# Kernel tuning notes

Measured on AMD Instinct MI355X. Metric: run time of the kernel, lower is better.

The kernel has to match this reference:

```python
import jax, jax.numpy as jnp
import numpy as np

DIM = 384
H = 6
D = DIM // H
MLP = 4 * DIM
SCALE = D ** -0.5
LN_EPS = 1e-5


def _ln(x, w, b):
    m = jnp.mean(x, axis=-1, keepdims=True)
    v = jnp.mean((x - m) ** 2, axis=-1, keepdims=True)
    return (x - m) * jax.lax.rsqrt(v + LN_EPS) * w + b


def setup_inputs() -> dict:
    key = jax.random.key(0)
    ks = jax.random.split(key, 8)
    B, N = 8, 1024
    x = jax.random.normal(ks[0], (B, N, DIM), dtype=jnp.float32)
    # torch nn.Linear weights are [out, in]
    qkv_w = jax.random.normal(ks[1], (3 * DIM, DIM), dtype=jnp.float32) * (DIM ** -0.5)
    proj_w = jax.random.normal(ks[2], (DIM, DIM), dtype=jnp.float32) * (DIM ** -0.5)
    proj_b = jnp.zeros((DIM,), jnp.float32)
    # L2Q params, 'quadratic' init
    alpha = jnp.full((H, 1, 1), 0.125, jnp.float32)
    beta = jnp.full((H, 1, 1), 0.5, jnp.float32)
    gamma = jnp.zeros((H, 1, 1), jnp.float32)
    ln1_w = jnp.ones((DIM,), jnp.float32)
    ln1_b = jnp.zeros((DIM,), jnp.float32)
    ln2_w = jnp.ones((DIM,), jnp.float32)
    ln2_b = jnp.zeros((DIM,), jnp.float32)
    w1 = jax.random.normal(ks[3], (MLP, DIM), dtype=jnp.float32) * (DIM ** -0.5)
    b1 = jnp.zeros((MLP,), jnp.float32)
    w2 = jax.random.normal(ks[4], (DIM, MLP), dtype=jnp.float32) * (MLP ** -0.5)
    b2 = jnp.zeros((DIM,), jnp.float32)
    return {"x": x, "qkv_w": qkv_w, "proj_w": proj_w, "proj_b": proj_b,
            "alpha": alpha, "beta": beta, "gamma": gamma,
            "ln1_w": ln1_w, "ln1_b": ln1_b, "ln2_w": ln2_w, "ln2_b": ln2_b,
            "w1": w1, "b1": b1, "w2": w2, "b2": b2}


def reference(x, qkv_w, proj_w, proj_b, alpha, beta, gamma,
              ln1_w, ln1_b, ln2_w, ln2_b, w1, b1, w2, b2):
    B, N, C = x.shape
    # --- L2Q attention on LN(x) ---
    h = _ln(x, ln1_w, ln1_b)
    qkv = (h @ qkv_w.T).reshape(B, N, 3, H, D)
    q = qkv[:, :, 0].transpose(0, 2, 1, 3)  # [B,H,N,D]
    k = qkv[:, :, 1].transpose(0, 2, 1, 3)
    v = qkv[:, :, 2].transpose(0, 2, 1, 3)
    logits = jnp.einsum('bhnd,bhmd->bhnm', q, k) * SCALE
    attn = jax.nn.relu(alpha * logits ** 2 + beta * logits + gamma)
    attn = attn / (jnp.sum(attn, axis=-1, keepdims=True) + 1e-6)
    out = jnp.einsum('bhnm,bhmd->bhnd', attn, v)
    out = out.transpose(0, 2, 1, 3).reshape(B, N, C)
    x = x + out @ proj_w.T + proj_b
    # --- MLP on LN(x), exact GELU (torch default) ---
    h2 = _ln(x, ln2_w, ln2_b)
    m = jax.nn.gelu(h2 @ w1.T + b1, approximate=False)
    x = x + m @ w2.T + b2
    return x
```

## Files before the change

kernel.cpp:

```cpp
#include <hip/hip_runtime.h>
#include <hip/hip_bf16.h>
#include <math.h>

#define DIMC 384
#define NH 6
#define HD 64
#define MLPD 1536
#define BS 8
#define SEQ 1024
#define T_TOK (BS*SEQ)
#define TC ((size_t)T_TOK*DIMC)
#define QK_SCALE 0.125f

typedef __bf16 bf16;
typedef bf16 bf16x4 __attribute__((ext_vector_type(4)));
typedef bf16 bf16x8 __attribute__((ext_vector_type(8)));
typedef float floatx4 __attribute__((ext_vector_type(4)));

__device__ __forceinline__ void async_cp16(const void* gsrc, void* ldst) {
    __builtin_amdgcn_global_load_lds(
        (const __attribute__((address_space(1))) unsigned int*)gsrc,
        (__attribute__((address_space(3))) unsigned int*)ldst,
        16, 0, 0);
}

__global__ __launch_bounds__(256)
void prep_kernel(const float* __restrict__ s0, const float* __restrict__ s1,
                 const float* __restrict__ s2, const float* __restrict__ s3,
                 bf16* __restrict__ dst,
                 const float* __restrict__ x, const float* __restrict__ lw,
                 const float* __restrict__ lb, bf16* __restrict__ out) {
    if (blockIdx.x < 1728) {
        int i = blockIdx.x * 256 + threadIdx.x;
        const int n0 = 110592, n1 = 36864, n2 = 147456;
        const float4* src; int j;
        if (i < n0)           { src = (const float4*)s0; j = i; }
        else if (i < n0+n1)   { src = (const float4*)s1; j = i - n0; }
        else if (i < n0+n1+n2){ src = (const float4*)s2; j = i - n0 - n1; }
        else                  { src = (const float4*)s3; j = i - n0 - n1 - n2; }
        float4 v = src[j];
        bf16x4 o; o[0] = (bf16)v.x; o[1] = (bf16)v.y; o[2] = (bf16)v.z; o[3] = (bf16)v.w;
        ((bf16x4*)dst)[i] = o;
    } else {
        int row = (blockIdx.x - 1728) * 4 + (threadIdx.x >> 6);
        int t = threadIdx.x & 63;
        const float* xr = x + (size_t)row * DIMC;
        float vals[6];
        float s = 0.f;
        #pragma unroll
        for (int i = 0; i < 6; i++) { vals[i] = xr[t + i*64]; s += vals[i]; }
        #pragma unroll
        for (int m = 32; m; m >>= 1) s += __shfl_xor(s, m);
        float mean = s * (1.0f / DIMC);
        float sq = 0.f;
        #pragma unroll
        for (int i = 0; i < 6; i++) { float d = vals[i] - mean; sq += d * d; }
        #pragma unroll
        for (int m = 32; m; m >>= 1) sq += __shfl_xor(sq, m);
        float rstd = rsqrtf(sq * (1.0f / DIMC) + 1e-5f);
        bf16* orow = out + (size_t)row * DIMC;
        #pragma unroll
        for (int i = 0; i < 6; i++) {
            int c = t + i*64;
            orow[c] = (bf16)((vals[i] - mean) * rstd * lw[c] + lb[c]);
        }
    }
}

__global__ __launch_bounds__(256)
void ln2_fused(const float* __restrict__ x, const bf16* __restrict__ p0,
               const bf16* __restrict__ p1, const float* __restrict__ pb,
               const float* __restrict__ w, const float* __restrict__ b,
               float* __restrict__ x1, bf16* __restrict__ h) {
    int row = blockIdx.x * 4 + (threadIdx.x >> 6);
    int t = threadIdx.x & 63;
    size_t base = (size_t)row * DIMC;
    float vals[6];
    float s = 0.f;
    #pragma unroll
    for (int i = 0; i < 6; i++) {
        int c = t + i*64;
        float v = x[base + c] + (float)p0[base + c] + (float)p1[base + c] + pb[c];
        vals[i] = v; s += v;
    }
    #pragma unroll
    for (int m = 32; m; m >>= 1) s += __shfl_xor(s, m);
    float mean = s * (1.0f / DIMC);
    float sq = 0.f;
    #pragma unroll
    for (int i = 0; i < 6; i++) { float d = vals[i] - mean; sq += d * d; }
    #pragma unroll
    for (int m = 32; m; m >>= 1) sq += __shfl_xor(sq, m);
    float rstd = rsqrtf(sq * (1.0f / DIMC) + 1e-5f);
    #pragma unroll
    for (int i = 0; i < 6; i++) {
        int c = t + i*64;
        x1[base + c] = vals[i];
        h[base + c] = (bf16)((vals[i] - mean) * rstd * w[c] + b[c]);
    }
}

__global__ __launch_bounds__(256)
void reduce4(float* __restrict__ xo, const bf16* __restrict__ p0, const bf16* __restrict__ p1,
             const bf16* __restrict__ p2, const bf16* __restrict__ p3,
             const float* __restrict__ b2) {
    int i = blockIdx.x * 256 + threadIdx.x;
    float4 v = ((const float4*)xo)[i];
    int c = (i % 96) * 4;
    float4 bb = *(const float4*)(b2 + c);
    bf16x4 a0 = ((const bf16x4*)p0)[i], a1 = ((const bf16x4*)p1)[i];
    bf16x4 a2 = ((const bf16x4*)p2)[i], a3 = ((const bf16x4*)p3)[i];
    v.x += bb.x + (float)a0[0] + (float)a1[0] + (float)a2[0] + (float)a3[0];
    v.y += bb.y + (float)a0[1] + (float)a1[1] + (float)a2[1] + (float)a3[1];
    v.z += bb.z + (float)a0[2] + (float)a1[2] + (float)a2[2] + (float)a3[2];
    v.w += bb.w + (float)a0[3] + (float)a1[3] + (float)a2[3] + (float)a3[3];
    ((float4*)xo)[i] = v;
}

enum { EPI_NONE = 0, EPI_QKV = 1, EPI_GELU = 3 };

template<int EPI, int K, int KS, typename OutT>
__global__ __launch_bounds__(256)
void gemm_bt(const bf16* __restrict__ A, const bf16* __restrict__ W,
             const float* __restrict__ bias, OutT* out, int M, int N) {
    __shared__ __align__(16) bf16 Ash[128*32];
    __shared__ __align__(16) bf16 Bsh[128*32];
    constexpr int KB = K / KS;
    int tid = threadIdx.x;
    int lane = tid & 63, w = tid >> 6;
    int quad = lane >> 4, l16 = lane & 15;
    int rbase = blockIdx.y * 128 + (w >> 1) * 64;
    int cbase = blockIdx.x * 128 + (w & 1) * 64;
    int kbase = blockIdx.z * KB;
    int c1 = w * 64 + lane;
    int c2 = c1 + 256;
    const bf16* Ag1 = A + (size_t)(blockIdx.y*128 + (c1 >> 2)) * K + kbase + (c1 & 3) * 8;
    const bf16* Ag2 = A + (size_t)(blockIdx.y*128 + (c2 >> 2)) * K + kbase + (c2 & 3) * 8;
    const bf16* Wg1 = W + (size_t)(blockIdx.x*128 + (c1 >> 2)) * K + kbase + (c1 & 3) * 8;
    const bf16* Wg2 = W + (size_t)(blockIdx.x*128 + (c2 >> 2)) * K + kbase + (c2 & 3) * 8;
    bf16* As1 = Ash + c1 * 8;  bf16* As2 = Ash + c2 * 8;
    bf16* Bs1 = Bsh + c1 * 8;  bf16* Bs2 = Bsh + c2 * 8;

    int arow = (w >> 1) * 64;
    int brow = (w & 1) * 64;
    floatx4 acc[4][4] = {};
    #pragma unroll
    for (int kk = 0; kk < KB / 32; kk++) {
        __syncthreads();
        async_cp16(Ag1 + kk*32, As1);
        async_cp16(Ag2 + kk*32, As2);
        async_cp16(Wg1 + kk*32, Bs1);
        async_cp16(Wg2 + kk*32, Bs2);
        __syncthreads();
        bf16x8 a[4], bfr[4];
        #pragma unroll
        for (int tm = 0; tm < 4; tm++)
            a[tm] = *(const bf16x8*)&Ash[(arow + tm*16 + l16) * 32 + quad*8];
        #pragma unroll
        for (int tn = 0; tn < 4; tn++)
            bfr[tn] = *(const bf16x8*)&Bsh[(brow + tn*16 + l16) * 32 + quad*8];
        #pragma unroll
        for (int tm = 0; tm < 4; tm++)
            #pragma unroll
            for (int tn = 0; tn < 4; tn++)
                acc[tm][tn] = __builtin_amdgcn_mfma_f32_16x16x32_bf16(a[tm], bfr[tn], acc[tm][tn], 0, 0, 0);
    }

    #pragma unroll
    for (int tm = 0; tm < 4; tm++)
        #pragma unroll
        for (int tn = 0; tn < 4; tn++) {
            if constexpr (EPI == EPI_QKV) {
                int colb = cbase + tn*16 + l16;
                int which = colb / 384;
                int rowb = rbase + tm*16 + quad*4;
                int bb = rowb >> 10;
                if (which == 2) {
                    int rem = colb - 768;
                    int hh = rem >> 6, d = rem & 63;
                    int n = rowb & 1023;
                    bf16x4 pk;
                    #pragma unroll
                    for (int r = 0; r < 4; r++) pk[r] = (bf16)acc[tm][tn][r];
                    *(bf16x4*)((bf16*)out + 2*TC + (((size_t)(bb*NH + hh) * HD + d) << 10) + n) = pk;
                } else {
                    int rem = colb - which*384;
                    int hh = rem >> 6, d = rem & 63;
                    #pragma unroll
                    for (int r = 0; r < 4; r++) {
                        int n = (rowb & 1023) + r;
                        ((bf16*)out)[(size_t)which*TC + (((size_t)(bb*NH + hh) * SEQ + n) << 6) + d]
                            = (bf16)acc[tm][tn][r];
                    }
                }
            } else if constexpr (EPI == EPI_NONE) {
                OutT* ob = out + (size_t)blockIdx.z * M * N;
                #pragma unroll
                for (int r = 0; r < 4; r++) {
                    int row = rbase + tm*16 + quad*4 + r;
                    int col = cbase + tn*16 + l16;
                    ob[(size_t)row * N + col] = (OutT)acc[tm][tn][r];
                }
            } else {
                #pragma unroll
                for (int r = 0; r < 4; r++) {
                    int row = rbase + tm*16 + quad*4 + r;
                    int col = cbase + tn*16 + l16;
                    float v = acc[tm][tn][r] + bias[col];
                    v = 0.5f * v * (1.0f + erff(v * 0.70710678118f));
                    out[(size_t)row * N + col] = (OutT)v;
                }
            }
        }
}

__global__ __launch_bounds__(256)
void attn_kernel(const bf16* __restrict__ q, const bf16* __restrict__ k,
                 const bf16* __restrict__ vt, const float* __restrict__ alpha,
                 const float* __restrict__ beta, const float* __restrict__ gamma,
                 bf16* __restrict__ attn_out) {
    __shared__ __align__(16) bf16 Psh[64][260];
    __shared__ float rsW[4][64];
    __shared__ float rs_final[64];

    int L = blockIdx.x;
    int xcd = L & 7, slot = L >> 3;
    int qt = slot & 15;
    int bh = xcd + ((slot >> 4) << 3);
    int bb = bh / NH, h = bh % NH;
    int q0 = qt * 64;
    int tid = threadIdx.x;
    int w = tid >> 6, lane = tid & 63, quad = lane >> 4, l16 = lane & 15;
    float av = alpha[h] * (QK_SCALE * QK_SCALE), bv = beta[h] * QK_SCALE, gv = gamma[h];
    const bf16* qb  = q  + (size_t)bh * SEQ * HD;
    const bf16* kb  = k  + (size_t)bh * SEQ * HD;
    const bf16* vtb = vt + (size_t)bh * HD * SEQ;

    floatx4 o[4] = {};
    float rsp[4] = {0.f, 0.f, 0.f, 0.f};

    bf16x8 kf[2][4], vf[8];
    #pragma unroll
    for (int ks = 0; ks < 2; ks++)
        #pragma unroll
        for (int ksub = 0; ksub < 4; ksub++)
            kf[ks][ksub] = *(const bf16x8*)(kb + (size_t)(w*64 + ksub*16 + l16) * HD + ks*32 + quad*8);
    const bf16* vrow = vtb + (size_t)(w*16 + l16) * SEQ;
    #pragma unroll
    for (int ksl = 0; ksl < 8; ksl++)
        vf[ksl] = *(const bf16x8*)(vrow + ksl*32 + quad*8);

    for (int c = 0; c < 4; c++) {
        #pragma unroll
        for (int qsub = 0; qsub < 4; qsub++) {
            bf16x8 qa0 = *(const bf16x8*)(qb + (size_t)(q0 + qsub*16 + l16) * HD + quad*8);
            bf16x8 qa1 = *(const bf16x8*)(qb + (size_t)(q0 + qsub*16 + l16) * HD + 32 + quad*8);
            floatx4 s[4] = {};
            #pragma unroll
            for (int ksub = 0; ksub < 4; ksub++)
                s[ksub] = __builtin_amdgcn_mfma_f32_16x16x32_bf16(kf[0][ksub], qa0, s[ksub], 0, 0, 0);
            #pragma unroll
            for (int ksub = 0; ksub < 4; ksub++)
                s[ksub] = __builtin_amdgcn_mfma_f32_16x16x32_bf16(kf[1][ksub], qa1, s[ksub], 0, 0, 0);
            #pragma unroll
            for (int ksub = 0; ksub < 4; ksub++) {
                bf16x4 p4;
                float rsum = 0.f;
                #pragma unroll
                for (int r = 0; r < 4; r++) {
                    float xx = s[ksub][r];
                    float p = fmaxf((av*xx + bv)*xx + gv, 0.f);
                    p4[r] = (bf16)p;
                    rsum += p;
                }
                rsp[qsub] += rsum;
                *(bf16x4*)&Psh[qsub*16 + l16][w*64 + ksub*16 + quad*4] = p4;
            }
        }
        __syncthreads();
        if (c < 3) {
            int kc = (c+1)*256 + w*64;
            #pragma unroll
            for (int ks = 0; ks < 2; ks++)
                #pragma unroll
                for (int ksub = 0; ksub < 4; ksub++)
                    kf[ks][ksub] = *(const bf16x8*)(kb + (size_t)(kc + ksub*16 + l16) * HD + ks*32 + quad*8);
        }
        #pragma unroll
        for (int ksl = 0; ksl < 8; ksl++) {
            #pragma unroll
            for (int qsub = 0; qsub < 4; qsub++) {
                bf16x4 plo = *(const bf16x4*)&Psh[qsub*16 + l16][ksl*32 + quad*8];
                bf16x4 phi = *(const bf16x4*)&Psh[qsub*16 + l16][ksl*32 + quad*8 + 4];
                bf16x8 pf = __builtin_shufflevector(plo, phi, 0, 1, 2, 3, 4, 5, 6, 7);
                o[qsub] = __builtin_amdgcn_mfma_f32_16x16x32_bf16(pf, vf[ksl], o[qsub], 0, 0, 0);
            }
        }
        if (c < 3) {
            const bf16* vr2 = vrow + (c+1)*256;
            #pragma unroll
            for (int ksl = 0; ksl < 8; ksl++)
                vf[ksl] = *(const bf16x8*)(vr2 + ksl*32 + quad*8);
        }
        __syncthreads();
    }

    #pragma unroll
    for (int qsub = 0; qsub < 4; qsub++) {
        rsp[qsub] += __shfl_xor(rsp[qsub], 16);
        rsp[qsub] += __shfl_xor(rsp[qsub], 32);
    }
    if (quad == 0) {
        #pragma unroll
        for (int qsub = 0; qsub < 4; qsub++)
            rsW[w][qsub*16 + l16] = rsp[qsub];
    }
    __syncthreads();
    if (tid < 64)
        rs_final[tid] = rsW[0][tid] + rsW[1][tid] + rsW[2][tid] + rsW[3][tid] + 1e-6f;
    __syncthreads();

    #pragma unroll
    for (int qsub = 0; qsub < 4; qsub++)
        #pragma unroll
        for (int r = 0; r < 4; r++) {
            int ql = qsub*16 + quad*4 + r;
            float rv = rs_final[ql];
            int n = q0 + ql;
            attn_out[((size_t)(bb*SEQ + n)) * DIMC + h*HD + w*16 + l16] =
                (bf16)(o[qsub][r] / rv);
        }
}

extern "C" void kernel_launch(void* const* d_in, const int* in_sizes, int n_in,
                              void* d_out, int out_size, void* d_ws, size_t ws_size,
                              hipStream_t stream) {
    const float* x      = (const float*)d_in[0];
    const float* qkv_w  = (const float*)d_in[1];
    const float* proj_w = (const float*)d_in[2];
    const float* proj_b = (const float*)d_in[3];
    const float* alpha  = (const float*)d_in[4];
    const float* beta   = (const float*)d_in[5];
    const float* gamma  = (const float*)d_in[6];
    const float* ln1_w  = (const float*)d_in[7];
    const float* ln1_b  = (const float*)d_in[8];
    const float* ln2_w  = (const float*)d_in[9];
    const float* ln2_b  = (const float*)d_in[10];
    const float* w1     = (const float*)d_in[11];
    const float* b1     = (const float*)d_in[12];
    const float* w2     = (const float*)d_in[13];
    const float* b2     = (const float*)d_in[14];
    float* out = (float*)d_out;

    char* base = (char*)d_ws;
    bf16* wq_bf = (bf16*)base;
    bf16* wp_bf = wq_bf + 442368;
    bf16* w1_bf = wq_bf + 589824;
    bf16* w2_bf = wq_bf + 1179648;
    bf16* h      = (bf16*)(base + 3538944);
    bf16* qkv    = (bf16*)(base + 9830400);
    bf16* attn_o = (bf16*)(base + 28704768);
    bf16* m      = qkv;
    bf16* Pp     = (bf16*)(base + 34996224);
    bf16* Pm     = (bf16*)(base + 34996224);

    prep_kernel<<<1728 + T_TOK/4, 256, 0, stream>>>(
        qkv_w, proj_w, w1, w2, wq_bf, x, ln1_w, ln1_b, h);
    gemm_bt<EPI_QKV, 384, 1, bf16><<<dim3(9, 64, 1), 256, 0, stream>>>(
        h, wq_bf, nullptr, qkv, T_TOK, 1152);
    attn_kernel<<<768, 256, 0, stream>>>(
        qkv, qkv + TC, qkv + 2*TC, alpha, beta, gamma, attn_o);
    gemm_bt<EPI_NONE, 384, 2, bf16><<<dim3(3, 64, 2), 256, 0, stream>>>(
        attn_o, wp_bf, nullptr, Pp, T_TOK, DIMC);
    ln2_fused<<<T_TOK/4, 256, 0, stream>>>(x, Pp, Pp + TC, proj_b, ln2_w, ln2_b, out, h);
    gemm_bt<EPI_GELU, 384, 1, bf16><<<dim3(12, 64, 1), 256, 0, stream>>>(
        h, w1_bf, b1, m, T_TOK, MLPD);
    gemm_bt<EPI_NONE, 1536, 4, bf16><<<dim3(3, 64, 4), 256, 0, stream>>>(
        m, w2_bf, nullptr, Pm, T_TOK, DIMC);
    reduce4<<<TC/4/256, 256, 0, stream>>>(out, Pm, Pm + TC, Pm + 2*TC, Pm + 3*TC, b2);
}
```

Baseline: 225.3 us.

## Halve attention query tile to 32 rows, doubling grid and splitting V loads

The attention kernel now handles 32 queries per block instead of 64, so the grid doubles to 1536 blocks. Q fragments are loaded once into registers and kept there, and the V fragments for the current chunk are loaded in two halves just before use instead of being prefetched a chunk ahead. This should raise occupancy and parallelism and cut register pressure. The cost is that each K/V chunk is reloaded by twice as many blocks and V load latency is less hidden.

```diff
diff --git a/kernel.cpp b/kernel.cpp
--- a/kernel.cpp
+++ b/kernel.cpp
@@ -219,16 +219,16 @@
                  const bf16* __restrict__ vt, const float* __restrict__ alpha,
                  const float* __restrict__ beta, const float* __restrict__ gamma,
                  bf16* __restrict__ attn_out) {
-    __shared__ __align__(16) bf16 Psh[64][260];
-    __shared__ float rsW[4][64];
-    __shared__ float rs_final[64];
+    __shared__ __align__(16) bf16 Psh[32][260];
+    __shared__ float rsW[4][32];
+    __shared__ float rs_final[32];
 
     int L = blockIdx.x;
     int xcd = L & 7, slot = L >> 3;
-    int qt = slot & 15;
-    int bh = xcd + ((slot >> 4) << 3);
+    int qt = slot & 31;
+    int bh = xcd + ((slot >> 5) << 3);
     int bb = bh / NH, h = bh % NH;
-    int q0 = qt * 64;
+    int q0 = qt * 32;
     int tid = threadIdx.x;
     int w = tid >> 6, lane = tid & 63, quad = lane >> 4, l16 = lane & 15;
     float av = alpha[h] * (QK_SCALE * QK_SCALE), bv = beta[h] * QK_SCALE, gv = gamma[h];
@@ -236,32 +236,34 @@
     const bf16* kb  = k  + (size_t)bh * SEQ * HD;
     const bf16* vtb = vt + (size_t)bh * HD * SEQ;
 
-    floatx4 o[4] = {};
-    float rsp[4] = {0.f, 0.f, 0.f, 0.f};
-
-    bf16x8 kf[2][4], vf[8];
+    floatx4 o[2] = {};
+    float rsp[2] = {0.f, 0.f};
+
+    bf16x8 qa[2][2];
+    #pragma unroll
+    for (int qsub = 0; qsub < 2; qsub++)
+        #pragma unroll
+        for (int ks = 0; ks < 2; ks++)
+            qa[qsub][ks] = *(const bf16x8*)(qb + (size_t)(q0 + qsub*16 + l16) * HD + ks*32 + quad*8);
+
+    bf16x8 kf[2][4], vfA[4], vfB[4];
     #pragma unroll
     for (int ks = 0; ks < 2; ks++)
         #pragma unroll
         for (int ksub = 0; ksub < 4; ksub++)
             kf[ks][ksub] = *(const bf16x8*)(kb + (size_t)(w*64 + ksub*16 + l16) * HD + ks*32 + quad*8);
     const bf16* vrow = vtb + (size_t)(w*16 + l16) * SEQ;
-    #pragma unroll
-    for (int ksl = 0; ksl < 8; ksl++)
-        vf[ksl] = *(const bf16x8*)(vrow + ksl*32 + quad*8);
 
     for (int c = 0; c < 4; c++) {
         #pragma unroll
-        for (int qsub = 0; qsub < 4; qsub++) {
-            bf16x8 qa0 = *(const bf16x8*)(qb + (size_t)(q0 + qsub*16 + l16) * HD + quad*8);
-            bf16x8 qa1 = *(const bf16x8*)(qb + (size_t)(q0 + qsub*16 + l16) * HD + 32 + quad*8);
+        for (int qsub = 0; qsub < 2; qsub++) {
             floatx4 s[4] = {};
             #pragma unroll
             for (int ksub = 0; ksub < 4; ksub++)
-                s[ksub] = __builtin_amdgcn_mfma_f32_16x16x32_bf16(kf[0][ksub], qa0, s[ksub], 0, 0, 0);
+                s[ksub] = __builtin_amdgcn_mfma_f32_16x16x32_bf16(kf[0][ksub], qa[qsub][0], s[ksub], 0, 0, 0);
             #pragma unroll
             for (int ksub = 0; ksub < 4; ksub++)
-                s[ksub] = __builtin_amdgcn_mfma_f32_16x16x32_bf16(kf[1][ksub], qa1, s[ksub], 0, 0, 0);
+                s[ksub] = __builtin_amdgcn_mfma_f32_16x16x32_bf16(kf[1][ksub], qa[qsub][1], s[ksub], 0, 0, 0);
             #pragma unroll
             for (int ksub = 0; ksub < 4; ksub++) {
                 bf16x4 p4;
@@ -277,6 +279,12 @@
                 *(bf16x4*)&Psh[qsub*16 + l16][w*64 + ksub*16 + quad*4] = p4;
             }
         }
+        {
+            const bf16* vr = vrow + c*256;
+            #pragma unroll
+            for (int ksl = 0; ksl < 4; ksl++)
+                vfA[ksl] = *(const bf16x8*)(vr + ksl*32 + quad*8);
+        }
         __syncthreads();
         if (c < 3) {
             int kc = (c+1)*256 + w*64;
@@ -286,42 +294,52 @@
                 for (int ksub = 0; ksub < 4; ksub++)
                     kf[ks][ksub] = *(const bf16x8*)(kb + (size_t)(kc + ksub*16 + l16) * HD + ks*32 + quad*8);
         }
-        #pragma unroll
-        for (int ksl = 0; ksl < 8; ksl++) {
-            #pragma unroll
-            for (int qsub = 0; qsub < 4; qsub++) {
+        {
+            const bf16* vr = vrow + c*256;
+            #pragma unroll
+            for (int ksl = 0; ksl < 4; ksl++)
+                vfB[ksl] = *(const bf16x8*)(vr + (ksl+4)*32 + quad*8);
+        }
+        #pragma unroll
+        for (int ksl = 0; ksl < 4; ksl++) {
+            #pragma unroll
+            for (int qsub = 0; qsub < 2; qsub++) {
                 bf16x4 plo = *(const bf16x4*)&Psh[qsub*16 + l16][ksl*32 + quad*8];
                 bf16x4 phi = *(const bf16x4*)&Psh[qsub*16 + l16][ksl*32 + quad*8 + 4];
                 bf16x8 pf = __builtin_shufflevector(plo, phi, 0, 1, 2, 3, 4, 5, 6, 7);
-                o[qsub] = __builtin_amdgcn_mfma_f32_16x16x32_bf16(pf, vf[ksl], o[qsub], 0, 0, 0);
+                o[qsub] = __builtin_amdgcn_mfma_f32_16x16x32_bf16(pf, vfA[ksl], o[qsub], 0, 0, 0);
             }
         }
-        if (c < 3) {
-            const bf16* vr2 = vrow + (c+1)*256;
-            #pragma unroll
-            for (int ksl = 0; ksl < 8; ksl++)
-                vf[ksl] = *(const bf16x8*)(vr2 + ksl*32 + quad*8);
+        #pragma unroll
+        for (int ksl = 0; ksl < 4; ksl++) {
+            #pragma unroll
+            for (int qsub = 0; qsub < 2; qsub++) {
+                bf16x4 plo = *(const bf16x4*)&Psh[qsub*16 + l16][(ksl+4)*32 + quad*8];
+                bf16x4 phi = *(const bf16x4*)&Psh[qsub*16 + l16][(ksl+4)*32 + quad*8 + 4];
+                bf16x8 pf = __builtin_shufflevector(plo, phi, 0, 1, 2, 3, 4, 5, 6, 7);
+                o[qsub] = __builtin_amdgcn_mfma_f32_16x16x32_bf16(pf, vfB[ksl], o[qsub], 0, 0, 0);
+            }
         }
         __syncthreads();
     }
 
     #pragma unroll
-    for (int qsub = 0; qsub < 4; qsub++) {
+    for (int qsub = 0; qsub < 2; qsub++) {
         rsp[qsub] += __shfl_xor(rsp[qsub], 16);
         rsp[qsub] += __shfl_xor(rsp[qsub], 32);
     }
     if (quad == 0) {
         #pragma unroll
-        for (int qsub = 0; qsub < 4; qsub++)
+        for (int qsub = 0; qsub < 2; qsub++)
             rsW[w][qsub*16 + l16] = rsp[qsub];
     }
     __syncthreads();
-    if (tid < 64)
+    if (tid < 32)
         rs_final[tid] = rsW[0][tid] + rsW[1][tid] + rsW[2][tid] + rsW[3][tid] + 1e-6f;
     __syncthreads();
 
     #pragma unroll
-    for (int qsub = 0; qsub < 4; qsub++)
+    for (int qsub = 0; qsub < 2; qsub++)
         #pragma unroll
         for (int r = 0; r < 4; r++) {
             int ql = qsub*16 + quad*4 + r;
@@ -368,7 +386,7 @@
         qkv_w, proj_w, w1, w2, wq_bf, x, ln1_w, ln1_b, h);
     gemm_bt<EPI_QKV, 384, 1, bf16><<<dim3(9, 64, 1), 256, 0, stream>>>(
         h, wq_bf, nullptr, qkv, T_TOK, 1152);
-    attn_kernel<<<768, 256, 0, stream>>>(
+    attn_kernel<<<1536, 256, 0, stream>>>(
         qkv, qkv + TC, qkv + 2*TC, alpha, beta, gamma, attn_o);
     gemm_bt<EPI_NONE, 384, 2, bf16><<<dim3(3, 64, 2), 256, 0, stream>>>(
         attn_o, wp_bf, nullptr, Pp, T_TOK, DIMC);
```

New measurement: 237.5 us. +5.4%, slower.

## Split attention keys across waves with 16-query tiles and register-resident P

Applied to the files above, without the earlier changes.

The attention kernel now processes 16 queries per block instead of 64, launching four times as many blocks. Each wave handles a quarter of the key range and feeds the probability tile straight from registers into the PV MFMA, using a permuted K row order so the score layout matches the A-operand. This removes the shared-memory P staging and the per-chunk barriers, and adds a cross-wave reduction of output and row sums through shared memory at the end. K and V are now reloaded from global memory by many more blocks, which raises global/L2 traffic.

```diff
diff --git a/kernel.cpp b/kernel.cpp
--- a/kernel.cpp
+++ b/kernel.cpp
@@ -219,16 +219,15 @@
                  const bf16* __restrict__ vt, const float* __restrict__ alpha,
                  const float* __restrict__ beta, const float* __restrict__ gamma,
                  bf16* __restrict__ attn_out) {
-    __shared__ __align__(16) bf16 Psh[64][260];
-    __shared__ float rsW[4][64];
-    __shared__ float rs_final[64];
+    __shared__ float Ored[4][16][68];
+    __shared__ float rsW[4][16];
 
     int L = blockIdx.x;
     int xcd = L & 7, slot = L >> 3;
-    int qt = slot & 15;
-    int bh = xcd + ((slot >> 4) << 3);
+    int qt = slot & 63;
+    int bh = xcd + ((slot >> 6) << 3);
     int bb = bh / NH, h = bh % NH;
-    int q0 = qt * 64;
+    int q0 = qt * 16;
     int tid = threadIdx.x;
     int w = tid >> 6, lane = tid & 63, quad = lane >> 4, l16 = lane & 15;
     float av = alpha[h] * (QK_SCALE * QK_SCALE), bv = beta[h] * QK_SCALE, gv = gamma[h];
@@ -236,100 +235,87 @@
     const bf16* kb  = k  + (size_t)bh * SEQ * HD;
     const bf16* vtb = vt + (size_t)bh * HD * SEQ;
 
+    bf16x8 qa[2];
+    #pragma unroll
+    for (int s = 0; s < 2; s++)
+        qa[s] = *(const bf16x8*)(qb + (size_t)(q0 + l16) * HD + s*32 + quad*8);
+
+    int krow0 = ((l16 >> 2) << 3) + (l16 & 3);
+
     floatx4 o[4] = {};
-    float rsp[4] = {0.f, 0.f, 0.f, 0.f};
-
-    bf16x8 kf[2][4], vf[8];
-    #pragma unroll
-    for (int ks = 0; ks < 2; ks++)
-        #pragma unroll
-        for (int ksub = 0; ksub < 4; ksub++)
-            kf[ks][ksub] = *(const bf16x8*)(kb + (size_t)(w*64 + ksub*16 + l16) * HD + ks*32 + quad*8);
-    const bf16* vrow = vtb + (size_t)(w*16 + l16) * SEQ;
-    #pragma unroll
-    for (int ksl = 0; ksl < 8; ksl++)
-        vf[ksl] = *(const bf16x8*)(vrow + ksl*32 + quad*8);
+    float rsp = 0.f;
+    int k0 = w * 256;
+
+    bf16x8 kf[2][2][2];
+    #pragma unroll
+    for (int s = 0; s < 2; s++)
+        #pragma unroll
+        for (int b = 0; b < 2; b++)
+            #pragma unroll
+            for (int j = 0; j < 2; j++)
+                kf[s][b][j] = *(const bf16x8*)(kb + (size_t)(k0 + b*32 + j*4 + krow0) * HD + s*32 + quad*8);
 
     for (int c = 0; c < 4; c++) {
-        #pragma unroll
-        for (int qsub = 0; qsub < 4; qsub++) {
-            bf16x8 qa0 = *(const bf16x8*)(qb + (size_t)(q0 + qsub*16 + l16) * HD + quad*8);
-            bf16x8 qa1 = *(const bf16x8*)(qb + (size_t)(q0 + qsub*16 + l16) * HD + 32 + quad*8);
-            floatx4 s[4] = {};
-            #pragma unroll
-            for (int ksub = 0; ksub < 4; ksub++)
-                s[ksub] = __builtin_amdgcn_mfma_f32_16x16x32_bf16(kf[0][ksub], qa0, s[ksub], 0, 0, 0);
-            #pragma unroll
-            for (int ksub = 0; ksub < 4; ksub++)
-                s[ksub] = __builtin_amdgcn_mfma_f32_16x16x32_bf16(kf[1][ksub], qa1, s[ksub], 0, 0, 0);
-            #pragma unroll
-            for (int ksub = 0; ksub < 4; ksub++) {
-                bf16x4 p4;
-                float rsum = 0.f;
+        int ck = k0 + c*64;
+        floatx4 sb[2][2] = {};
+        #pragma unroll
+        for (int s = 0; s < 2; s++)
+            #pragma unroll
+            for (int b = 0; b < 2; b++)
+                #pragma unroll
+                for (int j = 0; j < 2; j++)
+                    sb[b][j] = __builtin_amdgcn_mfma_f32_16x16x32_bf16(kf[s][b][j], qa[s], sb[b][j], 0, 0, 0);
+        if (c < 3) {
+            int nk = ck + 64;
+            #pragma unroll
+            for (int s = 0; s < 2; s++)
+                #pragma unroll
+                for (int b = 0; b < 2; b++)
+                    #pragma unroll
+                    for (int j = 0; j < 2; j++)
+                        kf[s][b][j] = *(const bf16x8*)(kb + (size_t)(nk + b*32 + j*4 + krow0) * HD + s*32 + quad*8);
+        }
+        bf16x8 vf[2][4];
+        #pragma unroll
+        for (int b = 0; b < 2; b++)
+            #pragma unroll
+            for (int d = 0; d < 4; d++)
+                vf[b][d] = *(const bf16x8*)(vtb + (size_t)(l16 + 16*d) * SEQ + ck + b*32 + quad*8);
+        bf16x8 pf[2];
+        #pragma unroll
+        for (int b = 0; b < 2; b++)
+            #pragma unroll
+            for (int j = 0; j < 2; j++)
                 #pragma unroll
                 for (int r = 0; r < 4; r++) {
-                    float xx = s[ksub][r];
+                    float xx = sb[b][j][r];
                     float p = fmaxf((av*xx + bv)*xx + gv, 0.f);
-                    p4[r] = (bf16)p;
-                    rsum += p;
+                    rsp += p;
+                    pf[b][j*4 + r] = (bf16)p;
                 }
-                rsp[qsub] += rsum;
-                *(bf16x4*)&Psh[qsub*16 + l16][w*64 + ksub*16 + quad*4] = p4;
-            }
-        }
-        __syncthreads();
-        if (c < 3) {
-            int kc = (c+1)*256 + w*64;
-            #pragma unroll
-            for (int ks = 0; ks < 2; ks++)
-                #pragma unroll
-                for (int ksub = 0; ksub < 4; ksub++)
-                    kf[ks][ksub] = *(const bf16x8*)(kb + (size_t)(kc + ksub*16 + l16) * HD + ks*32 + quad*8);
-        }
-        #pragma unroll
-        for (int ksl = 0; ksl < 8; ksl++) {
-            #pragma unroll
-            for (int qsub = 0; qsub < 4; qsub++) {
-                bf16x4 plo = *(const bf16x4*)&Psh[qsub*16 + l16][ksl*32 + quad*8];
-                bf16x4 phi = *(const bf16x4*)&Psh[qsub*16 + l16][ksl*32 + quad*8 + 4];
-                bf16x8 pf = __builtin_shufflevector(plo, phi, 0, 1, 2, 3, 4, 5, 6, 7);
-                o[qsub] = __builtin_amdgcn_mfma_f32_16x16x32_bf16(pf, vf[ksl], o[qsub], 0, 0, 0);
-            }
-        }
-        if (c < 3) {
-            const bf16* vr2 = vrow + (c+1)*256;
-            #pragma unroll
-            for (int ksl = 0; ksl < 8; ksl++)
-                vf[ksl] = *(const bf16x8*)(vr2 + ksl*32 + quad*8);
-        }
-        __syncthreads();
-    }
-
-    #pragma unroll
-    for (int qsub = 0; qsub < 4; qsub++) {
-        rsp[qsub] += __shfl_xor(rsp[qsub], 16);
-        rsp[qsub] += __shfl_xor(rsp[qsub], 32);
-    }
-    if (quad == 0) {
-        #pragma unroll
-        for (int qsub = 0; qsub < 4; qsub++)
-            rsW[w][qsub*16 + l16] = rsp[qsub];
-    }
+        #pragma unroll
+        for (int b = 0; b < 2; b++)
+            #pragma unroll
+            for (int d = 0; d < 4; d++)
+                o[d] = __builtin_amdgcn_mfma_f32_16x16x32_bf16(pf[b], vf[b][d], o[d], 0, 0, 0);
+    }
+
+    rsp += __shfl_xor(rsp, 16);
+    rsp += __shfl_xor(rsp, 32);
+    if (quad == 0) rsW[w][l16] = rsp;
+    #pragma unroll
+    for (int d = 0; d < 4; d++)
+        #pragma unroll
+        for (int r = 0; r < 4; r++)
+            Ored[w][quad*4 + r][l16 + 16*d] = o[d][r];
     __syncthreads();
-    if (tid < 64)
-        rs_final[tid] = rsW[0][tid] + rsW[1][tid] + rsW[2][tid] + rsW[3][tid] + 1e-6f;
-    __syncthreads();
-
-    #pragma unroll
-    for (int qsub = 0; qsub < 4; qsub++)
-        #pragma unroll
-        for (int r = 0; r < 4; r++) {
-            int ql = qsub*16 + quad*4 + r;
-            float rv = rs_final[ql];
-            int n = q0 + ql;
-            attn_out[((size_t)(bb*SEQ + n)) * DIMC + h*HD + w*16 + l16] =
-                (bf16)(o[qsub][r] / rv);
-        }
+    #pragma unroll
+    for (int qq = 0; qq < 4; qq++) {
+        int qp = w*4 + qq;
+        float rt = rsW[0][qp] + rsW[1][qp] + rsW[2][qp] + rsW[3][qp] + 1e-6f;
+        float v = Ored[0][qp][lane] + Ored[1][qp][lane] + Ored[2][qp][lane] + Ored[3][qp][lane];
+        attn_out[((size_t)(bb*SEQ + q0 + qp)) * DIMC + h*HD + lane] = (bf16)(v / rt);
+    }
 }
 
 extern "C" void kernel_launch(void* const* d_in, const int* in_sizes, int n_in,
@@ -368,7 +354,7 @@
         qkv_w, proj_w, w1, w2, wq_bf, x, ln1_w, ln1_b, h);
     gemm_bt<EPI_QKV, 384, 1, bf16><<<dim3(9, 64, 1), 256, 0, stream>>>(
         h, wq_bf, nullptr, qkv, T_TOK, 1152);
-    attn_kernel<<<768, 256, 0, stream>>>(
+    attn_kernel<<<3072, 256, 0, stream>>>(
         qkv, qkv + TC, qkv + 2*TC, alpha, beta, gamma, attn_o);
     gemm_bt<EPI_NONE, 384, 2, bf16><<<dim3(3, 64, 2), 256, 0, stream>>>(
         attn_o, wp_bf, nullptr, Pp, T_TOK, DIMC);
```

Result: slower. 276.0 us (+22.5%).
